# Optimization experiments

Measured on AMD Instinct MI355X. Metric: run time of the kernel, lower is better.

## Reference

```python
import jax, jax.numpy as jnp
import numpy as np

PRE_NMS_THRESH = 0.05
PRE_NMS_TOP_N = 200
NMS_THRESH = 0.5
FPN_POST_NMS_TOP_N = 100
MIN_SIZE = 0.0
NUM_CLASSES = 2
C = NUM_CLASSES - 1
NB = 2
STRIDES = (8, 16, 32, 64, 128)
HS = (100, 50, 25, 13, 7)
WS = (128, 64, 32, 16, 8)
IMG_H, IMG_W = 800, 1024
MAXV = 8  # max #vertices of quad-clipped-by-quad polygon


def _shoelace_fixed(V, n):
    # area of polygon stored in fixed buffer V[MAXV,2] with n valid vertices
    a = jnp.asarray(0.0, V.dtype)
    for k in range(MAXV):
        nxt = jnp.where(jnp.equal(k, n - 1), 0, k + 1)
        term = V[k, 0] * V[nxt, 1] - V[nxt, 0] * V[k, 1]
        a = a + jnp.where(k < n, term, 0.0)
    return 0.5 * jnp.abs(a)


def _quad_area(Q):  # Q: [4,2]
    x, y = Q[:, 0], Q[:, 1]
    return 0.5 * jnp.abs(jnp.sum(x * jnp.roll(y, -1) - jnp.roll(x, -1) * y))


def _clip_halfplane(V, n, p1, p2, orient):
    # Sutherland-Hodgman clip of polygon (V,n) against directed edge p1->p2
    d = p2 - p1

    def side(p):
        return orient * (d[0] * (p[1] - p1[1]) - d[1] * (p[0] - p1[0]))

    out = jnp.zeros((MAXV, 2), V.dtype)
    cnt = jnp.int32(0)
    for k in range(MAXV):
        cur = V[k]
        prev = V[jnp.where(jnp.equal(k, 0), n - 1, k - 1)]
        sc = side(cur)
        sp = side(prev)
        cur_in = sc >= 0.0
        prev_in = sp >= 0.0
        denom = sp - sc
        t = sp / jnp.where(jnp.abs(denom) > 1e-9, denom, 1e-9)
        ip = prev + t * (cur - prev)
        valid = k < n
        emit_ip = valid & (cur_in != prev_in)
        out = jnp.where(emit_ip, out.at[cnt].set(ip, mode='drop'), out)
        cnt = cnt + emit_ip.astype(jnp.int32)
        emit_cur = valid & cur_in
        out = jnp.where(emit_cur, out.at[cnt].set(cur, mode='drop'), out)
        cnt = cnt + emit_cur.astype(jnp.int32)
    return out, cnt


def _poly_inter_area(A, B):  # A,B: [4,2] convex quads
    sB = jnp.sum(B[:, 0] * jnp.roll(B[:, 1], -1) - jnp.roll(B[:, 0], -1) * B[:, 1])
    orient = jnp.where(sB >= 0.0, 1.0, -1.0)
    V = jnp.zeros((MAXV, 2), A.dtype).at[:4].set(A)
    n = jnp.int32(4)
    for e in range(4):
        V, n = _clip_halfplane(V, n, B[e], B[(e + 1) % 4], orient)
    return _shoelace_fixed(V, n)


def _process_level(loc, cls_l, reg_l, image_sizes):
    Nb, Cc, H, W = cls_l.shape
    # (N,C,H,W) -> (N,HW*C) with index = (h*W+w)*C + c (matches permute/reshape)
    scores = jax.nn.sigmoid(cls_l.transpose(0, 2, 3, 1).reshape(Nb, H * W * Cc))
    cand = scores > PRE_NMS_THRESH
    masked = jnp.where(cand, scores, 0.0)
    k = min(PRE_NMS_TOP_N, H * W * Cc)
    vals, idx = jax.lax.top_k(masked, k)
    loc_idx = idx // Cc
    labels = idx % Cc + 1
    regr = reg_l.transpose(0, 2, 3, 1).reshape(Nb, H * W, 8)
    reg_g = jnp.take_along_axis(regr, loc_idx[..., None], axis=1)  # [Nb,k,8]
    loc_g = loc[loc_idx]  # [Nb,k,2]
    poly = jnp.tile(loc_g, (1, 1, 4)) - reg_g  # (x-r0, y-r1, ..., x-r6, y-r7)
    hh = image_sizes[:, 0].astype(poly.dtype)[:, None, None]
    ww = image_sizes[:, 1].astype(poly.dtype)[:, None, None]
    xs = jnp.clip(poly[..., 0::2], 0.0, ww - 1.0)
    ys = jnp.clip(poly[..., 1::2], 0.0, hh - 1.0)
    poly = jnp.stack([xs, ys], axis=-1).reshape(Nb, k, 8)
    valid = vals > PRE_NMS_THRESH
    bw = xs.max(-1) - xs.min(-1)
    bh = ys.max(-1) - ys.min(-1)
    valid = valid & (bw >= MIN_SIZE) & (bh >= MIN_SIZE)
    sc = jnp.where(valid, jnp.sqrt(vals), 0.0)
    return poly, sc, labels, valid


def _nms_single(poly, scores, labels, valid):
    T = scores.shape[0]
    order = jnp.argsort(-scores)
    poly = poly[order]
    scores = scores[order]
    labels = labels[order]
    valid = valid[order]
    quads = poly.reshape(T, 4, 2)

    def pairwise_iou(q):
        inter = jax.vmap(jax.vmap(_poly_inter_area, (None, 0)), (0, None))(q, q)
        areas = jax.vmap(_quad_area)(q)
        union = areas[:, None] + areas[None, :] - inter
        return inter / jnp.maximum(union, 1e-9)

    # IoU only feeds boolean suppression decisions -> no gradient flows through it
    iou = jax.lax.stop_gradient(pairwise_iou(quads))
    ar = jnp.arange(T)

    def body(i, keep):
        sup = (iou[i] > NMS_THRESH) & (ar > i)
        return jnp.where(keep[i], keep & ~sup, keep)

    keep = jax.lax.stop_gradient(jax.lax.fori_loop(0, T, body, valid))
    final = jnp.where(keep, scores, -1.0)
    top_s, top_i = jax.lax.top_k(final, FPN_POST_NMS_TOP_N)
    ok = top_s > 0.0
    return poly[top_i], jnp.where(ok, top_s, 0.0), labels[top_i], ok


def _forward(locs, clss, regs, image_sizes):
    parts = [_process_level(l, c, r, image_sizes) for l, c, r in zip(locs, clss, regs)]
    poly = jnp.concatenate([p[0] for p in parts], axis=1)
    sc = jnp.concatenate([p[1] for p in parts], axis=1)
    lab = jnp.concatenate([p[2] for p in parts], axis=1)
    val = jnp.concatenate([p[3] for p in parts], axis=1)
    return jax.vmap(_nms_single)(poly, sc, lab, val)


def setup_inputs() -> dict:
    key = jax.random.key(0)
    inp = {}
    k = key
    for i, (h, w, s) in enumerate(zip(HS, WS, STRIDES)):
        k, k1, k2, k3 = jax.random.split(k, 4)
        sx = jnp.arange(w, dtype=jnp.float32) * s + s // 2
        sy = jnp.arange(h, dtype=jnp.float32) * s + s // 2
        yy, xx = jnp.meshgrid(sy, sx, indexing='ij')
        inp[f'locations_l{i}'] = jnp.stack([xx.reshape(-1), yy.reshape(-1)], axis=1)
        inp[f'box_cls_l{i}'] = jax.random.normal(k1, (NB, C, h, w), dtype=jnp.float32)
        inp[f'box_reg_l{i}'] = jax.random.normal(k2, (NB, 8, h, w), dtype=jnp.float32) * (2.0 * s)
        inp[f'centerness_l{i}'] = jax.random.normal(k3, (NB, 1, h, w), dtype=jnp.float32)
    inp['image_sizes'] = jnp.array([[IMG_H, IMG_W]] * NB, dtype=jnp.int32)
    return inp


def reference(locations_l0, locations_l1, locations_l2, locations_l3, locations_l4,
              box_cls_l0, box_cls_l1, box_cls_l2, box_cls_l3, box_cls_l4,
              box_reg_l0, box_reg_l1, box_reg_l2, box_reg_l3, box_reg_l4,
              centerness_l0, centerness_l1, centerness_l2, centerness_l3, centerness_l4,
              image_sizes):
    # centerness is accepted but unused, matching the original module's forward
    locs = [locations_l0, locations_l1, locations_l2, locations_l3, locations_l4]
    clss = [box_cls_l0, box_cls_l1, box_cls_l2, box_cls_l3, box_cls_l4]
    regs = [box_reg_l0, box_reg_l1, box_reg_l2, box_reg_l3, box_reg_l4]
    boxes, scores, labels, valid = _forward(locs, clss, regs, image_sizes)
    return boxes, scores, labels, valid
```

## Files before the change

kernel.cpp:

```cpp
#include <hip/hip_runtime.h>

#pragma clang fp contract(off)

#define T_CAND 856
#define NW 14
#define NSH 16
#define HSTR 513

__device__ const int d_HW[5]  = {12800, 3200, 800, 208, 56};
__device__ const int d_K[5]   = {200, 200, 200, 200, 56};
__device__ const int d_OFF[5] = {0, 200, 400, 600, 800};

struct LevelPtrs {
  const float* loc[5];
  const float* cls[5];
  const float* reg[5];
  const int*   img;
};

__device__ __forceinline__ unsigned long long readlane64(unsigned long long v, int lane) {
  const unsigned lo = (unsigned)__builtin_amdgcn_readlane((int)(unsigned)(v & 0xFFFFFFFFULL), lane);
  const unsigned hi = (unsigned)__builtin_amdgcn_readlane((int)(unsigned)(v >> 32), lane);
  return ((unsigned long long)hi << 32) | lo;
}
__device__ __forceinline__ unsigned long long rfl64(unsigned long long v) {
  const unsigned lo = (unsigned)__builtin_amdgcn_readfirstlane((int)(unsigned)(v & 0xFFFFFFFFULL));
  const unsigned hi = (unsigned)__builtin_amdgcn_readfirstlane((int)(unsigned)(v >> 32));
  return ((unsigned long long)hi << 32) | lo;
}

__global__ __launch_bounds__(1024) void topk_kernel(LevelPtrs P,
    float* __restrict__ candPoly, float* __restrict__ candSc, unsigned* __restrict__ candValid) {
  __shared__ unsigned hist[NSH * HSTR];
  __shared__ unsigned histT[512];
  __shared__ __align__(16) unsigned long long gbuf[1024];
  __shared__ float mcache[12800];
  __shared__ int gcount;
  __shared__ int cutB;
  const int blk = blockIdx.x;
  const int b = blk / 5, l = blk % 5;
  const int HW = d_HW[l], K = d_K[l], OFF = d_OFF[l];
  const float* cls = P.cls[l] + (size_t)b * HW;
  const float* reg = P.reg[l] + (size_t)b * 8 * HW;
  const float* loc = P.loc[l];
  const int tid = threadIdx.x;

  for (int t = tid; t < NSH * HSTR; t += 1024) hist[t] = 0u;
  if (tid == 0) gcount = 0;
  __syncthreads();

  const int sh = (tid >> 2) & (NSH - 1);
  for (int idx = tid; idx < HW; idx += 1024) {
    const float x = cls[idx];
    const float s = (float)(1.0 / (1.0 + exp(-(double)x)));
    const float m = (s > 0.05f) ? s : 0.0f;
    mcache[idx] = m;
    atomicAdd(&hist[sh * HSTR + (__float_as_uint(m) >> 21)], 1u);
  }
  __syncthreads();
  for (int t = tid; t < 512; t += 1024) {
    unsigned sum = 0;
#pragma unroll
    for (int h = 0; h < NSH; ++h) sum += hist[h * HSTR + t];
    histT[t] = sum;
  }
  __syncthreads();
  if (tid == 0) {
    int acc = 0, bx = 511;
    for (; bx >= 0; --bx) { acc += (int)histT[bx]; if (acc >= K) break; }
    cutB = (bx < 0) ? 0 : bx;
  }
  __syncthreads();

  const int cb = cutB;
  for (int idx = tid; idx < HW; idx += 1024) {
    const unsigned kb = __float_as_uint(mcache[idx]);
    if ((int)(kb >> 21) >= cb) {
      const int pos = atomicAdd(&gcount, 1);
      if (pos < 1024)
        gbuf[pos] = ((unsigned long long)kb << 32)
                  | (unsigned long long)(0xFFFFFFFFu - (unsigned)idx);
    }
  }
  __syncthreads();
  const int G = min(gcount, 1024);
  if (tid < 4 && G + tid < 1024) gbuf[G + tid] = 0ULL;
  __syncthreads();

  if (tid < G) {
    const unsigned long long my = gbuf[tid];
    const int G4 = (G + 3) & ~3;
    int rank = 0;
    const ulonglong2* g2 = (const ulonglong2*)gbuf;
    for (int j = 0; j < G4 / 2; j += 2) {
      const ulonglong2 a = g2[j], c = g2[j + 1];
      rank += (a.x > my) ? 1 : 0;
      rank += (a.y > my) ? 1 : 0;
      rank += (c.x > my) ? 1 : 0;
      rank += (c.y > my) ? 1 : 0;
    }
    if (rank < K) {
      const float val = __uint_as_float((unsigned)(my >> 32));
      const int idx = (int)(0xFFFFFFFFu - (unsigned)(my & 0xFFFFFFFFULL));
      const float hh = (float)P.img[b * 2 + 0];
      const float ww = (float)P.img[b * 2 + 1];
      const float xmax = ww - 1.0f, ymax = hh - 1.0f;
      const float lx = loc[idx * 2 + 0], ly = loc[idx * 2 + 1];
      const int go = b * T_CAND + OFF + rank;
#pragma unroll
      for (int q = 0; q < 4; ++q) {
        const float rx = reg[(2 * q + 0) * HW + idx];
        const float ry = reg[(2 * q + 1) * HW + idx];
        const float pxv = fminf(fmaxf(lx - rx, 0.0f), xmax);
        const float pyv = fminf(fmaxf(ly - ry, 0.0f), ymax);
        candPoly[go * 8 + 2 * q + 0] = pxv;
        candPoly[go * 8 + 2 * q + 1] = pyv;
      }
      const bool v = (val > 0.05f);
      candSc[go]    = v ? sqrtf(val) : 0.0f;
      candValid[go] = v ? 1u : 0u;
    }
  }
}

__global__ __launch_bounds__(1024) void sort_kernel(
    const float* __restrict__ candPoly, const float* __restrict__ candSc,
    const unsigned* __restrict__ candValid,
    float* __restrict__ sPoly, float* __restrict__ sSc, unsigned* __restrict__ sValid,
    float* __restrict__ sAABB, unsigned* __restrict__ pairCount) {
  __shared__ __align__(16) unsigned long long key[T_CAND];
  const int b = blockIdx.x, tid = threadIdx.x;
  if (b == 0 && tid == 0) *pairCount = 0u;
  float sc = 0.0f;
  if (tid < T_CAND) {
    sc = candSc[b * T_CAND + tid];
    key[tid] = ((unsigned long long)__float_as_uint(sc) << 32)
             | (unsigned long long)(0xFFFFFFFFu - (unsigned)tid);
  }
  __syncthreads();
  if (tid < T_CAND) {
    const unsigned long long my = key[tid];
    int rank = 0;
    const ulonglong2* k2 = (const ulonglong2*)key;
    for (int j = 0; j < T_CAND / 2; j += 2) {
      const ulonglong2 a = k2[j], c = k2[j + 1];
      rank += (a.x > my) ? 1 : 0;
      rank += (a.y > my) ? 1 : 0;
      rank += (c.x > my) ? 1 : 0;
      rank += (c.y > my) ? 1 : 0;
    }
    sSc[b * T_CAND + rank]    = sc;
    sValid[b * T_CAND + rank] = candValid[b * T_CAND + tid];
    const float4* src = (const float4*)(candPoly + (size_t)(b * T_CAND + tid) * 8);
    const float4 s0 = src[0], s1 = src[1];
    float4* dst = (float4*)(sPoly + (size_t)(b * T_CAND + rank) * 8);
    dst[0] = s0;
    dst[1] = s1;
    float4 bb;
    bb.x = fminf(fminf(s0.x, s0.z), fminf(s1.x, s1.z));
    bb.y = fminf(fminf(s0.y, s0.w), fminf(s1.y, s1.w));
    bb.z = fmaxf(fmaxf(s0.x, s0.z), fmaxf(s1.x, s1.z));
    bb.w = fmaxf(fmaxf(s0.y, s0.w), fmaxf(s1.y, s1.w));
    *(float4*)(sAABB + (size_t)(b * T_CAND + rank) * 4) = bb;
  }
}

__global__ __launch_bounds__(64) void aabb_pairs_kernel(
    const float* __restrict__ sAABB, const unsigned* __restrict__ sValid,
    unsigned long long* __restrict__ MT, unsigned* __restrict__ pairList,
    unsigned* __restrict__ pairCount) {
  const int jt = blockIdx.x, it = blockIdx.y, b = blockIdx.z;
  const int lane = threadIdx.x;
  const int iRow = it * 64 + lane;
  if (jt < it) {
    if (iRow < T_CAND) MT[((size_t)b * NW + jt) * T_CAND + iRow] = 0ULL;
    return;
  }
  const int j = jt * 64 + lane;
  const int jc = j < T_CAND ? j : T_CAND - 1;
  const float4 jb = *(const float4*)(sAABB + (size_t)(b * T_CAND + jc) * 4);
  const bool jv = (j < T_CAND) && (sValid[b * T_CAND + j] != 0u);
  const int ic = iRow < T_CAND ? iRow : T_CAND - 1;
  const float4 ib = *(const float4*)(sAABB + (size_t)(b * T_CAND + ic) * 4);
  const int iv = (iRow < T_CAND) && (sValid[b * T_CAND + ic] != 0u);
  unsigned long long roww = 0ULL;
  for (int q = 0; q < 64; ++q) {
    const float iminx = __shfl(ib.x, q), iminy = __shfl(ib.y, q);
    const float imaxx = __shfl(ib.z, q), imaxy = __shfl(ib.w, q);
    const int ivq = __shfl(iv, q);
    const int irow_q = it * 64 + q;
    const bool ov = !(imaxx < jb.x || jb.z < iminx || imaxy < jb.y || jb.w < iminy);
    const bool pred = ivq && jv && (j > irow_q) && ov;
    const unsigned long long w = __ballot(pred);
    if (lane == q) roww = w;
  }
  if (iRow < T_CAND) MT[((size_t)b * NW + jt) * T_CAND + iRow] = 0ULL;
  const int cnt = __popcll(roww);
  int incl = cnt;
#pragma unroll
  for (int d = 1; d < 64; d <<= 1) {
    const int v = __shfl_up(incl, d);
    if (lane >= d) incl += v;
  }
  const int ex = incl - cnt;
  int base = 0;
  if (lane == 63) base = (int)atomicAdd(pairCount, (unsigned)incl);
  base = __shfl(base, 63);
  unsigned off = (unsigned)(base + ex);
  unsigned long long t = roww;
  while (t) {
    const int jb2 = (int)__builtin_ctzll(t);
    t &= t - 1;
    pairList[off++] = ((unsigned)b << 20) | ((unsigned)iRow << 10) | (unsigned)(jt * 64 + jb2);
  }
}

__global__ __launch_bounds__(256) void clip_kernel(
    const unsigned* __restrict__ pairList, const unsigned* __restrict__ pairCount,
    const float* __restrict__ sPoly, unsigned long long* __restrict__ MT) {
  __shared__ float VX[2][8][256];
  __shared__ float VY[2][8][256];
  const int tid = threadIdx.x;
  const unsigned count = *pairCount;
  for (unsigned t0 = blockIdx.x * 256 + tid; t0 < count; t0 += gridDim.x * 256) {
    const unsigned pk = pairList[t0];
    const int b = (pk >> 20) & 1, i = (pk >> 10) & 1023, j = pk & 1023;
    const float4* Ap4 = (const float4*)(sPoly + (size_t)(b * T_CAND + i) * 8);
    const float4 a01 = Ap4[0], a23 = Ap4[1];
    const float ax0 = a01.x, ay0 = a01.y, ax1 = a01.z, ay1 = a01.w,
                ax2 = a23.x, ay2 = a23.y, ax3 = a23.z, ay3 = a23.w;
    const float4* Bp4 = (const float4*)(sPoly + (size_t)(b * T_CAND + j) * 8);
    const float4 b01 = Bp4[0], b23 = Bp4[1];
    const float bx0 = b01.x, by0 = b01.y, bx1 = b01.z, by1 = b01.w,
                bx2 = b23.x, by2 = b23.y, bx3 = b23.z, by3 = b23.w;
    float sB = bx0 * by1 - bx1 * by0;
    sB += bx1 * by2 - bx2 * by1;
    sB += bx2 * by3 - bx3 * by2;
    sB += bx3 * by0 - bx0 * by3;
    const float orient = (sB >= 0.0f) ? 1.0f : -1.0f;

    VX[0][0][tid] = ax0; VY[0][0][tid] = ay0;
    VX[0][1][tid] = ax1; VY[0][1][tid] = ay1;
    VX[0][2][tid] = ax2; VY[0][2][tid] = ay2;
    VX[0][3][tid] = ax3; VY[0][3][tid] = ay3;
    int n = 4;
    const float bex[5] = {bx0, bx1, bx2, bx3, bx0};
    const float bey[5] = {by0, by1, by2, by3, by0};
#pragma unroll
    for (int e = 0; e < 4; ++e) {
      const int src = e & 1, dst = src ^ 1;
      const float p1x = bex[e], p1y = bey[e];
      const float dx = bex[e + 1] - p1x, dy = bey[e + 1] - p1y;
      int cnt = 0;
      int pidx = n - 1;
      pidx = pidx < 0 ? 0 : (pidx > 7 ? 7 : pidx);
      float px = VX[src][pidx][tid], py = VY[src][pidx][tid];
      float sp = orient * (dx * (py - p1y) - dy * (px - p1x));
      for (int k = 0; k < 8; ++k) {
        if (k >= n) break;
        const float cx = VX[src][k][tid], cy = VY[src][k][tid];
        const float sc2 = orient * (dx * (cy - p1y) - dy * (cx - p1x));
        const bool cin = (sc2 >= 0.0f), pin = (sp >= 0.0f);
        const float denom = sp - sc2;
        const float dd = (fabsf(denom) > 1e-9f) ? denom : 1e-9f;
        const float t = sp / dd;
        const float ipx = px + t * (cx - px);
        const float ipy = py + t * (cy - py);
        const bool e1 = (cin != pin);
        if (e1 && cnt < 8) { VX[dst][cnt][tid] = ipx; VY[dst][cnt][tid] = ipy; }
        cnt += e1 ? 1 : 0;
        if (cin && cnt < 8) { VX[dst][cnt][tid] = cx; VY[dst][cnt][tid] = cy; }
        cnt += cin ? 1 : 0;
        px = cx; py = cy; sp = sc2;
      }
      n = cnt;
    }
    float a = 0.0f;
    for (int k = 0; k < 8; ++k) {
      if (k >= n) break;
      const int nxt = (k == n - 1) ? 0 : ((k + 1 > 7) ? 7 : (k + 1));
      const float xk = VX[0][k][tid], yk = VY[0][k][tid];
      const float xn = VX[0][nxt][tid], yn = VY[0][nxt][tid];
      a += xk * yn - xn * yk;
    }
    const float inter = 0.5f * fabsf(a);
    float aA = ax0 * ay1 - ax1 * ay0;
    aA += ax1 * ay2 - ax2 * ay1;
    aA += ax2 * ay3 - ax3 * ay2;
    aA += ax3 * ay0 - ax0 * ay3;
    const float areaA = 0.5f * fabsf(aA);
    const float areaB = 0.5f * fabsf(sB);
    const float uni = areaA + areaB - inter;
    const float iou = inter / fmaxf(uni, 1e-9f);
    if (iou > 0.5f)
      atomicOr(&MT[((size_t)b * NW + (j >> 6)) * T_CAND + i], 1ULL << (j & 63));
  }
}

__global__ __launch_bounds__(1024) void nms_resolve_emit_kernel(
    const unsigned long long* __restrict__ MT, const unsigned* __restrict__ sValid,
    const float* __restrict__ sPoly, const float* __restrict__ sSc, float* __restrict__ out) {
  __shared__ __align__(16) unsigned long long mt[NW * T_CAND];
  __shared__ unsigned long long vb[16];
  __shared__ unsigned long long kw[NW];
  const int b = blockIdx.x;
  const int tid = threadIdx.x;
  const int wave = tid >> 6, lane = tid & 63;

  {
    const ulonglong2* g2 = (const ulonglong2*)(MT + (size_t)b * NW * T_CAND);
    ulonglong2* l2 = (ulonglong2*)mt;
    for (int t = tid; t < NW * T_CAND / 2; t += 1024) l2[t] = g2[t];
  }
  if (wave < NW) {
    const int idx = wave * 64 + lane;
    const bool v = (idx < T_CAND) && (sValid[b * T_CAND + idx] != 0u);
    const unsigned long long ball = __ballot(v);
    if (lane == 0) vb[wave] = ball;
  }
  __syncthreads();

  if (wave == 0) {
    unsigned long long kwreg = 0ULL;
    for (int q = 0; q < NW; ++q) {
      const unsigned long long* col = &mt[q * T_CAND];
      const int nrow = q * 64 + lane;
      const unsigned long long sup = col[nrow < T_CAND ? nrow : (T_CAND - 1)];
      unsigned long long acc = 0ULL;
      for (int wp = 0; wp < q; ++wp) {
        const unsigned long long row = col[wp * 64 + lane];
        const unsigned long long kword = readlane64(kwreg, wp);
        acc |= ((kword >> lane) & 1ULL) ? row : 0ULL;
      }
#pragma unroll
      for (int m = 1; m < 64; m <<= 1)
        acc |= (unsigned long long)__shfl_xor((long long)acc, m, 64);
      const unsigned long long S = rfl64(acc);
      const unsigned long long validq = rfl64(vb[q]);
      unsigned long long alive = validq & ~S;
      const unsigned long long suppr = __ballot(sup != 0ULL);
      unsigned long long rem = alive & suppr;
      while (rem) {
        const int s = (int)__builtin_ctzll(rem);
        rem &= rem - 1;
        if ((alive >> s) & 1ULL) {
          alive &= ~readlane64(sup, s);
          rem &= alive;
        }
      }
      if (lane == q) kwreg = alive;
    }
    if (lane < NW) kw[lane] = kwreg;
  }
  __syncthreads();

  if (tid < 100) {
    const int o = tid;
    int totalKeep = 0;
    for (int w = 0; w < NW; ++w) totalKeep += __popcll(kw[w]);
    const bool kept = o < totalKeep;
    int idx = 0;
    if (kept) {
      int r = o, w = 0;
      unsigned long long word = 0ULL;
      for (; w < NW; ++w) {
        word = kw[w];
        const int c = __popcll(word);
        if (r < c) break;
        r -= c;
      }
      for (int p = 0; p < r; ++p) word &= word - 1;
      idx = w * 64 + (__ffsll(word) - 1);
    } else {
      int r = o - totalKeep, w = 0;
      unsigned long long word = 0ULL;
      for (; w < NW; ++w) {
        const unsigned long long mk = (w == NW - 1) ? ((1ULL << (T_CAND - 64 * (NW - 1))) - 1ULL)
                                                    : ~0ULL;
        word = (~kw[w]) & mk;
        const int c = __popcll(word);
        if (r < c) break;
        r -= c;
      }
      for (int p = 0; p < r; ++p) word &= word - 1;
      idx = w * 64 + (__ffsll(word) - 1);
    }
    const float4* pp = (const float4*)(sPoly + (size_t)(b * T_CAND + idx) * 8);
    float4* ob2 = (float4*)(out + (size_t)b * 800 + (size_t)o * 8);
    ob2[0] = pp[0];
    ob2[1] = pp[1];
    out[1600 + b * 100 + o] = kept ? sSc[b * T_CAND + idx] : 0.0f;
    out[1800 + b * 100 + o] = 1.0f;
    out[2000 + b * 100 + o] = kept ? 1.0f : 0.0f;
  }
}

extern "C" void kernel_launch(void* const* d_in, const int* in_sizes, int n_in,
                              void* d_out, int out_size, void* d_ws, size_t ws_size,
                              hipStream_t stream) {
  (void)n_in; (void)out_size; (void)ws_size;
  LevelPtrs P;
  const bool interleaved = (in_sizes[2] == 204800);
  for (int l = 0; l < 5; ++l) {
    if (interleaved) {
      P.loc[l] = (const float*)d_in[4 * l + 0];
      P.cls[l] = (const float*)d_in[4 * l + 1];
      P.reg[l] = (const float*)d_in[4 * l + 2];
    } else {
      P.loc[l] = (const float*)d_in[l];
      P.cls[l] = (const float*)d_in[5 + l];
      P.reg[l] = (const float*)d_in[10 + l];
    }
  }
  P.img = (const int*)d_in[20];

  char* ws = (char*)d_ws;
  float*    candPoly  = (float*)(ws + 0);
  float*    candSc    = (float*)(ws + 54784);
  unsigned* candValid = (unsigned*)(ws + 61632);
  float*    sPoly     = (float*)(ws + 68480);
  float*    sSc       = (float*)(ws + 123264);
  unsigned* sValid    = (unsigned*)(ws + 130112);
  unsigned long long* MT = (unsigned long long*)(ws + 136960);
  float*    sAABB     = (float*)(ws + 328704);
  unsigned* pairCount = (unsigned*)(ws + 356096);
  unsigned* pairList  = (unsigned*)(ws + 356112);

  topk_kernel<<<dim3(10), dim3(1024), 0, stream>>>(P, candPoly, candSc, candValid);
  sort_kernel<<<dim3(2), dim3(1024), 0, stream>>>(candPoly, candSc, candValid,
                                                  sPoly, sSc, sValid, sAABB, pairCount);
  aabb_pairs_kernel<<<dim3(NW, NW, 2), dim3(64), 0, stream>>>(sAABB, sValid, MT,
                                                              pairList, pairCount);
  clip_kernel<<<dim3(512), dim3(256), 0, stream>>>(pairList, pairCount, sPoly, MT);
  nms_resolve_emit_kernel<<<dim3(2), dim3(1024), 0, stream>>>(MT, sValid, sPoly, sSc,
                                                              (float*)d_out);
}
```

Before: 75.11 us.

## Fuse AABB pair filtering into sort kernel and parallelize top-k cutoff scan

Merges the separate AABB pair-generation kernel into the sort kernel, so sorted boxes and validity bits stay in shared memory and one kernel launch plus a global round trip are removed. The pairCount reset moves into the top-k kernel. The serial single-thread histogram cutoff scan is replaced with a wave-wide prefix scan. In exchange, the pair work now runs on only two blocks of 16 waves instead of a 14x14x2 grid, which reduces parallelism for that stage.

Result: slower. 144.2 us (+92.0%).

```diff
diff --git a/kernel.cpp b/kernel.cpp
--- a/kernel.cpp
+++ b/kernel.cpp
@@ -30,7 +30,8 @@
 }
 
 __global__ __launch_bounds__(1024) void topk_kernel(LevelPtrs P,
-    float* __restrict__ candPoly, float* __restrict__ candSc, unsigned* __restrict__ candValid) {
+    float* __restrict__ candPoly, float* __restrict__ candSc, unsigned* __restrict__ candValid,
+    unsigned* __restrict__ pairCount) {
   __shared__ unsigned hist[NSH * HSTR];
   __shared__ unsigned histT[512];
   __shared__ __align__(16) unsigned long long gbuf[1024];
@@ -44,7 +45,9 @@
   const float* reg = P.reg[l] + (size_t)b * 8 * HW;
   const float* loc = P.loc[l];
   const int tid = threadIdx.x;
-
+  const int wave = tid >> 6, lane = tid & 63;
+
+  if (blk == 0 && tid == 0) *pairCount = 0u;
   for (int t = tid; t < NSH * HSTR; t += 1024) hist[t] = 0u;
   if (tid == 0) gcount = 0;
   __syncthreads();
@@ -65,10 +68,29 @@
     histT[t] = sum;
   }
   __syncthreads();
-  if (tid == 0) {
-    int acc = 0, bx = 511;
-    for (; bx >= 0; --bx) { acc += (int)histT[bx]; if (acc >= K) break; }
-    cutB = (bx < 0) ? 0 : bx;
+  if (wave == 0) {
+    const int t0 = lane * 8;
+    int h[8], loc8[8];
+#pragma unroll
+    for (int k = 0; k < 8; ++k) h[k] = (int)histT[t0 + k];
+    int run = 0;
+#pragma unroll
+    for (int k = 7; k >= 0; --k) { run += h[k]; loc8[k] = run; }
+    int v = run;
+#pragma unroll
+    for (int d = 1; d < 64; d <<= 1) {
+      const int u = __shfl_down(v, d);
+      if (lane + d < 64) v += u;
+    }
+    const int excl = v - run;
+    int cand = -1;
+#pragma unroll
+    for (int k = 7; k >= 0; --k)
+      if (cand < 0 && excl + loc8[k] >= K) cand = t0 + k;
+    const unsigned long long bal = __ballot(cand >= 0);
+    const int hi = 63 - __builtin_clzll(bal);
+    const int cb = __shfl(cand, hi);
+    if (lane == 0) cutB = cb;
   }
   __syncthreads();
 
@@ -123,20 +145,26 @@
   }
 }
 
-__global__ __launch_bounds__(1024) void sort_kernel(
+__global__ __launch_bounds__(1024) void sort_aabb_kernel(
     const float* __restrict__ candPoly, const float* __restrict__ candSc,
     const unsigned* __restrict__ candValid,
     float* __restrict__ sPoly, float* __restrict__ sSc, unsigned* __restrict__ sValid,
-    float* __restrict__ sAABB, unsigned* __restrict__ pairCount) {
+    unsigned long long* __restrict__ MT, unsigned* __restrict__ pairList,
+    unsigned* __restrict__ pairCount) {
   __shared__ __align__(16) unsigned long long key[T_CAND];
+  __shared__ __align__(16) float4 aabbL[T_CAND];
+  __shared__ unsigned char validL[NW * 64];
+  __shared__ unsigned long long vbits[NW];
   const int b = blockIdx.x, tid = threadIdx.x;
-  if (b == 0 && tid == 0) *pairCount = 0u;
+  const int wave = tid >> 6, lane = tid & 63;
+
   float sc = 0.0f;
   if (tid < T_CAND) {
     sc = candSc[b * T_CAND + tid];
     key[tid] = ((unsigned long long)__float_as_uint(sc) << 32)
              | (unsigned long long)(0xFFFFFFFFu - (unsigned)tid);
   }
+  if (tid >= T_CAND && tid < NW * 64) validL[tid] = 0;
   __syncthreads();
   if (tid < T_CAND) {
     const unsigned long long my = key[tid];
@@ -149,8 +177,10 @@
       rank += (c.x > my) ? 1 : 0;
       rank += (c.y > my) ? 1 : 0;
     }
+    const unsigned vfl = candValid[b * T_CAND + tid];
     sSc[b * T_CAND + rank]    = sc;
-    sValid[b * T_CAND + rank] = candValid[b * T_CAND + tid];
+    sValid[b * T_CAND + rank] = vfl;
+    validL[rank] = (unsigned char)vfl;
     const float4* src = (const float4*)(candPoly + (size_t)(b * T_CAND + tid) * 8);
     const float4 s0 = src[0], s1 = src[1];
     float4* dst = (float4*)(sPoly + (size_t)(b * T_CAND + rank) * 8);
@@ -161,57 +191,57 @@
     bb.y = fminf(fminf(s0.y, s0.w), fminf(s1.y, s1.w));
     bb.z = fmaxf(fmaxf(s0.x, s0.z), fmaxf(s1.x, s1.z));
     bb.w = fmaxf(fmaxf(s0.y, s0.w), fmaxf(s1.y, s1.w));
-    *(float4*)(sAABB + (size_t)(b * T_CAND + rank) * 4) = bb;
-  }
-}
-
-__global__ __launch_bounds__(64) void aabb_pairs_kernel(
-    const float* __restrict__ sAABB, const unsigned* __restrict__ sValid,
-    unsigned long long* __restrict__ MT, unsigned* __restrict__ pairList,
-    unsigned* __restrict__ pairCount) {
-  const int jt = blockIdx.x, it = blockIdx.y, b = blockIdx.z;
-  const int lane = threadIdx.x;
-  const int iRow = it * 64 + lane;
-  if (jt < it) {
-    if (iRow < T_CAND) MT[((size_t)b * NW + jt) * T_CAND + iRow] = 0ULL;
-    return;
-  }
-  const int j = jt * 64 + lane;
-  const int jc = j < T_CAND ? j : T_CAND - 1;
-  const float4 jb = *(const float4*)(sAABB + (size_t)(b * T_CAND + jc) * 4);
-  const bool jv = (j < T_CAND) && (sValid[b * T_CAND + j] != 0u);
-  const int ic = iRow < T_CAND ? iRow : T_CAND - 1;
-  const float4 ib = *(const float4*)(sAABB + (size_t)(b * T_CAND + ic) * 4);
-  const int iv = (iRow < T_CAND) && (sValid[b * T_CAND + ic] != 0u);
-  unsigned long long roww = 0ULL;
-  for (int q = 0; q < 64; ++q) {
-    const float iminx = __shfl(ib.x, q), iminy = __shfl(ib.y, q);
-    const float imaxx = __shfl(ib.z, q), imaxy = __shfl(ib.w, q);
-    const int ivq = __shfl(iv, q);
-    const int irow_q = it * 64 + q;
-    const bool ov = !(imaxx < jb.x || jb.z < iminx || imaxy < jb.y || jb.w < iminy);
-    const bool pred = ivq && jv && (j > irow_q) && ov;
-    const unsigned long long w = __ballot(pred);
-    if (lane == q) roww = w;
-  }
-  if (iRow < T_CAND) MT[((size_t)b * NW + jt) * T_CAND + iRow] = 0ULL;
-  const int cnt = __popcll(roww);
-  int incl = cnt;
-#pragma unroll
-  for (int d = 1; d < 64; d <<= 1) {
-    const int v = __shfl_up(incl, d);
-    if (lane >= d) incl += v;
-  }
-  const int ex = incl - cnt;
-  int base = 0;
-  if (lane == 63) base = (int)atomicAdd(pairCount, (unsigned)incl);
-  base = __shfl(base, 63);
-  unsigned off = (unsigned)(base + ex);
-  unsigned long long t = roww;
-  while (t) {
-    const int jb2 = (int)__builtin_ctzll(t);
-    t &= t - 1;
-    pairList[off++] = ((unsigned)b << 20) | ((unsigned)iRow << 10) | (unsigned)(jt * 64 + jb2);
+    aabbL[rank] = bb;
+  }
+  __syncthreads();
+  {
+    ulonglong2* m2 = (ulonglong2*)(MT + (size_t)b * NW * T_CAND);
+    const ulonglong2 z = {0ULL, 0ULL};
+    for (int t = tid; t < NW * T_CAND / 2; t += 1024) m2[t] = z;
+  }
+  if (wave < NW) {
+    const unsigned long long ball = __ballot(validL[wave * 64 + lane] != 0);
+    if (lane == 0) vbits[wave] = ball;
+  }
+  __syncthreads();
+
+  for (int t = wave; t < (NW * (NW + 1)) / 2; t += 16) {
+    int it = 0, rem = t;
+    while (rem >= NW - it) { rem -= NW - it; ++it; }
+    const int jt = it + rem;
+    const int j = jt * 64 + lane;
+    const bool jv = ((vbits[jt] >> lane) & 1ULL) != 0ULL;
+    const float4 jb = aabbL[j < T_CAND ? j : (T_CAND - 1)];
+    unsigned long long roww = 0ULL;
+    const unsigned long long ivb = vbits[it];
+    for (int q = 0; q < 64; ++q) {
+      const int irow = it * 64 + q;
+      const float4 ib = aabbL[irow < T_CAND ? irow : (T_CAND - 1)];
+      const bool iv = ((ivb >> q) & 1ULL) != 0ULL;
+      const bool ov = !(ib.z < jb.x || jb.z < ib.x || ib.w < jb.y || jb.w < ib.y);
+      const bool pred = iv && jv && (j > irow) && ov;
+      const unsigned long long w = __ballot(pred);
+      if (lane == q) roww = w;
+    }
+    const int cnt = __popcll(roww);
+    int incl = cnt;
+#pragma unroll
+    for (int d = 1; d < 64; d <<= 1) {
+      const int v = __shfl_up(incl, d);
+      if (lane >= d) incl += v;
+    }
+    const int ex = incl - cnt;
+    int base = 0;
+    if (lane == 63 && incl > 0) base = (int)atomicAdd(pairCount, (unsigned)incl);
+    base = __shfl(base, 63);
+    unsigned off = (unsigned)(base + ex);
+    unsigned long long tb = roww;
+    const int iRow = it * 64 + lane;
+    while (tb) {
+      const int jb2 = (int)__builtin_ctzll(tb);
+      tb &= tb - 1;
+      pairList[off++] = ((unsigned)b << 20) | ((unsigned)iRow << 10) | (unsigned)(jt * 64 + jb2);
+    }
   }
 }
 
@@ -422,15 +452,13 @@
   float*    sSc       = (float*)(ws + 123264);
   unsigned* sValid    = (unsigned*)(ws + 130112);
   unsigned long long* MT = (unsigned long long*)(ws + 136960);
-  float*    sAABB     = (float*)(ws + 328704);
-  unsigned* pairCount = (unsigned*)(ws + 356096);
-  unsigned* pairList  = (unsigned*)(ws + 356112);
-
-  topk_kernel<<<dim3(10), dim3(1024), 0, stream>>>(P, candPoly, candSc, candValid);
-  sort_kernel<<<dim3(2), dim3(1024), 0, stream>>>(candPoly, candSc, candValid,
-                                                  sPoly, sSc, sValid, sAABB, pairCount);
-  aabb_pairs_kernel<<<dim3(NW, NW, 2), dim3(64), 0, stream>>>(sAABB, sValid, MT,
-                                                              pairList, pairCount);
+  unsigned* pairCount = (unsigned*)(ws + 328704);
+  unsigned* pairList  = (unsigned*)(ws + 328720);
+
+  topk_kernel<<<dim3(10), dim3(1024), 0, stream>>>(P, candPoly, candSc, candValid, pairCount);
+  sort_aabb_kernel<<<dim3(2), dim3(1024), 0, stream>>>(candPoly, candSc, candValid,
+                                                       sPoly, sSc, sValid, MT,
+                                                       pairList, pairCount);
   clip_kernel<<<dim3(512), dim3(256), 0, stream>>>(pairList, pairCount, sPoly, MT);
   nms_resolve_emit_kernel<<<dim3(2), dim3(1024), 0, stream>>>(MT, sValid, sPoly, sSc,
                                                               (float*)d_out);
```
